# Performance work log

Hardware: AMD Instinct MI355X
Metric: run time of the kernel (lower is better)

The kernel has to match this reference:

```python
import jax, jax.numpy as jnp
import numpy as np

DEGREE = 2
STEPS = 7
N_FEATURES = 120
R_TARGETS = 4
LATENT = 4
D = N_FEATURES + R_TARGETS + LATENT          # 128: padded state dim
N_POLY = 1 + D + D * D                       # 16513: sum_{k=0..degree} D^k for degree=2
BATCH = 16384
W_SCALE = 1e-4                               # keep the iterated quadratic map stable


def setup_inputs() -> dict:
    key = jax.random.key(0)
    k1, k2 = jax.random.split(key)
    X = jax.random.normal(k1, (BATCH, N_FEATURES), dtype=jnp.float32)
    W = jax.random.normal(k2, (N_POLY, D), dtype=jnp.float32) * W_SCALE
    t_init = jnp.zeros((R_TARGETS,), dtype=jnp.float32)
    l_init = jnp.zeros((LATENT,), dtype=jnp.float32)
    return {"X": X, "W": W, "t_init": t_init, "l_init": l_init}


def _poly_full(x):
    """PolynomialFeatures via repeated outer products: [1, x, vec(x xp_{k-1}^T), ...]."""
    n = x.shape[0]
    xp = [jnp.ones((n, 1), x.dtype), x]
    for _ in range(2, DEGREE + 1):
        # [n, D, 1] * [n, 1, P] -> [n, D*P]  (matches tf: X @ expand_dims(XP[-1],1))
        xp.append((x[:, :, None] * xp[-1][:, None, :]).reshape(n, -1))
    return jnp.concatenate(xp, axis=-1)  # [n, N_POLY]


def reference(X, W, t_init, l_init):
    # pad inputs with r_targets + latent_units zeros, then add init values
    inits = jnp.concatenate([jnp.zeros((N_FEATURES,), X.dtype), t_init, l_init])
    x0 = jnp.pad(X, ((0, 0), (0, R_TARGETS + LATENT))) + inits  # [B, D]

    def step(x, _):
        return x + _poly_full(x) @ W, None  # TaylorMap: residual + poly GEMM

    x, _ = jax.lax.scan(step, x0, None, length=STEPS)
    # self._targets = target_features + appended extra target dims
    return x[:, N_FEATURES:N_FEATURES + R_TARGETS]  # [B, n_targets]
```

## Files before the change

### kernel.cpp

```cpp
#include <hip/hip_runtime.h>
#include <hip/hip_bf16.h>


#define DSTATE 128
#define BATCH  16384
#define NSTEPS 7
#define BT     64
#define NSL    585

typedef __attribute__((ext_vector_type(8)))  short  short8;
typedef __attribute__((ext_vector_type(16))) float  f32x16;

__device__ __forceinline__ unsigned short f2bf(float f){
    unsigned int u = __float_as_uint(f);
    u += 0x7fff + ((u >> 16) & 1);
    return (unsigned short)(u >> 16);
}

__global__ void prep_kernel(const float* __restrict__ W, short8* __restrict__ A){
    int gid = blockIdx.x * 256 + threadIdx.x;
    const int ntotal = 4 * 130 * 8 * 64;
    if (gid >= ntotal) return;
    int lane = gid & 63; int r = gid >> 6;
    int s = r & 7;  r >>= 3;
    int row = r % 130;
    int t   = r / 130;
    int d  = t * 32 + (lane & 31);
    int kb = (lane >> 5) * 8;
    int dst;
    bool zero = false;
    if (row < 64){
        int sl = row >> 4;
        if (s < sl) return;
        dst = t * NSL + 9 * row + (s - sl);
    } else if (row < 128){
        int p  = 127 - row;
        int sl = row >> 4;
        if (s < sl) return;
        int ca = 8 - (p >> 4);
        dst = t * NSL + 9 * p + ca + (s - sl);
    } else if (row == 128){
        dst = t * NSL + 576 + s;
    } else {
        if (s) return;
        dst = t * NSL + 584;
        zero = true;
    }
    union { short8 v; unsigned short u[8]; } fr;
#pragma unroll
    for (int e = 0; e < 8; ++e){
        int j = s * 16 + kb + e;
        float v;
        if (zero) v = 0.0f;
        else if (row < 128){
            if      (j < row)  v = 0.0f;
            else if (j == row) v = W[(129 + 128 * row + j) * 128 + d];
            else               v = W[(129 + 128 * row + j) * 128 + d]
                                 + W[(129 + 128 * j + row) * 128 + d];
        } else {
            v = W[(1 + j) * 128 + d];
        }
        fr.u[e] = f2bf(v);
    }
    A[(size_t)dst * 64 + lane] = fr.v;
}

__global__ __launch_bounds__(512)
void taylor_kernel(const float* __restrict__ X, const float* __restrict__ W,
                   const float* __restrict__ tini, const float* __restrict__ lini,
                   const short8* __restrict__ A, float* __restrict__ out)
{
    __shared__ float  x_lds[DSTATE * BT];
    __shared__ float  w0_lds[DSTATE];
    __shared__ short8 bpack[2 * 8 * 64];
    __shared__ float  sc_lds[2][4 * 64 * 17];

    const int tid  = threadIdx.x;
    const int lane = tid & 63;
    const int w    = tid >> 6;
    const int t    = w & 3;
    const int g    = w >> 2;
    const int ln   = lane & 31;
    const int hi   = lane >> 5;
    const int b0   = blockIdx.x * BT;

#pragma unroll
    for (int it = 0; it < 16; ++it){
        int entry = tid + it * 512;
        int b = entry >> 7, d = entry & 127;
        float v;
        if      (d < 120) v = X[(b0 + b) * 120 + d];
        else if (d < 124) v = tini[d - 120];
        else              v = lini[d - 124];
        x_lds[d * BT + b] = v;
    }
    if (tid < DSTATE) w0_lds[tid] = W[tid];

    const short8* const Aw = A + ((size_t)t * NSL + (size_t)g * 288) * 64 + lane;
    const f32x16 zero16 = {};

#pragma unroll 1
    for (int step = 0; step < NSTEPS; ++step){
        __syncthreads();

        const bool active = (step < NSTEPS - 1) || (t == 3);

        const short8* ap = Aw;
        short8 abuf[9];
        if (active){
#pragma unroll
            for (int s = 0; s < 9; ++s) abuf[s] = ap[s * 64];
            ap += 9 * 64;
        }

#pragma unroll
        for (int f0 = 0; f0 < 2; ++f0){
            int f  = tid + f0 * 512;
            int gg = f >> 9, s = (f >> 6) & 7, l = f & 63;
            int c  = gg * 32 + (l & 31);
            int jb = 16 * s + 8 * (l >> 5);
            union { short8 v; unsigned short u[8]; } fr;
#pragma unroll
            for (int e = 0; e < 8; ++e)
                fr.u[e] = f2bf(x_lds[(jb + e) * BT + c]);
            bpack[f] = fr.v;
        }

        f32x16 acc0, acc1;
        if (active){
            if (g == 0){
#pragma unroll
                for (int r = 0; r < 16; ++r){
                    int d = 32 * t + (r & 3) + 8 * (r >> 2) + 4 * hi;
                    acc0[r] = x_lds[d * BT + ln]      + w0_lds[d];
                    acc1[r] = x_lds[d * BT + 32 + ln] + w0_lds[d];
                }
            } else {
#pragma unroll
                for (int r = 0; r < 16; ++r){ acc0[r] = 0.f; acc1[r] = 0.f; }
            }
        }

        __syncthreads();

        if (active){
            short8 bfrag0[8], bfrag1[8];

#define PAIRS(BK)                                                               \
            {                                                                   \
                _Pragma("unroll")                                               \
                for (int s = 0; s < 8 - (BK); ++s){                             \
                    bfrag0[s] = bpack[((BK) + s) * 64 + lane];                  \
                    bfrag1[s] = bpack[512 + ((BK) + s) * 64 + lane];            \
                }                                                               \
                _Pragma("unroll 2")                                             \
                for (int q = 0; q < 16; ++q){                                   \
                    const int p = 16 * (BK) + q;                                \
                    float s0a = x_lds[p * BT + ln];                             \
                    float s0b = x_lds[p * BT + 32 + ln];                        \
                    float s1a = x_lds[(127 - p) * BT + ln];                     \
                    float s1b = x_lds[(127 - p) * BT + 32 + ln];                \
                    f32x16 Y0, Y1;                                              \
                    _Pragma("unroll")                                           \
                    for (int s = 0; s < 8 - (BK); ++s){                         \
                        Y0 = __builtin_amdgcn_mfma_f32_32x32x16_bf16(abuf[s], bfrag0[s], s ? Y0 : zero16, 0, 0, 0); \
                        Y1 = __builtin_amdgcn_mfma_f32_32x32x16_bf16(abuf[s], bfrag1[s], s ? Y1 : zero16, 0, 0, 0); \
                        abuf[s] = ap[s * 64];                                   \
                    }                                                           \
                    acc0 += s0a * Y0;                                           \
                    acc1 += s0b * Y1;                                           \
                    f32x16 Z0, Z1;                                              \
                    _Pragma("unroll")                                           \
                    for (int s = 0; s < 1 + (BK); ++s){                         \
                        Z0 = __builtin_amdgcn_mfma_f32_32x32x16_bf16(abuf[8 - (BK) + s], bfrag0[7 - 2 * (BK) + s], s ? Z0 : zero16, 0, 0, 0); \
                        Z1 = __builtin_amdgcn_mfma_f32_32x32x16_bf16(abuf[8 - (BK) + s], bfrag1[7 - 2 * (BK) + s], s ? Z1 : zero16, 0, 0, 0); \
                        abuf[8 - (BK) + s] = ap[(8 - (BK) + s) * 64];           \
                    }                                                           \
                    acc0 += s1a * Z0;                                           \
                    acc1 += s1b * Z1;                                           \
                    ap += 9 * 64;                                               \
                }                                                               \
            }

            if (g == 0){
                PAIRS(0) PAIRS(1)
            } else {
                PAIRS(2) PAIRS(3)
#pragma unroll
                for (int s = 0; s < 8; ++s){
                    bfrag0[s] = bpack[s * 64 + lane];
                    bfrag1[s] = bpack[512 + s * 64 + lane];
                }
#pragma unroll
                for (int s = 0; s < 8; ++s){
                    acc0 = __builtin_amdgcn_mfma_f32_32x32x16_bf16(abuf[s], bfrag0[s], acc0, 0, 0, 0);
                    acc1 = __builtin_amdgcn_mfma_f32_32x32x16_bf16(abuf[s], bfrag1[s], acc1, 0, 0, 0);
                }
#pragma unroll
                for (int r = 0; r < 16; ++r){
                    sc_lds[0][(t * 64 + lane) * 17 + r] = acc0[r];
                    sc_lds[1][(t * 64 + lane) * 17 + r] = acc1[r];
                }
            }
#undef PAIRS
        }

        __syncthreads();
        if (active && g == 0){
#pragma unroll
            for (int r = 0; r < 16; ++r){
                acc0[r] += sc_lds[0][(t * 64 + lane) * 17 + r];
                acc1[r] += sc_lds[1][(t * 64 + lane) * 17 + r];
            }
            if (step < NSTEPS - 1){
#pragma unroll
                for (int r = 0; r < 16; ++r){
                    int d = 32 * t + (r & 3) + 8 * (r >> 2) + 4 * hi;
                    x_lds[d * BT + ln]      = acc0[r];
                    x_lds[d * BT + 32 + ln] = acc1[r];
                }
            } else if (hi == 0){
                *(float4*)(out + (size_t)(b0 + ln) * 4) =
                    make_float4(acc0[12], acc0[13], acc0[14], acc0[15]);
                *(float4*)(out + (size_t)(b0 + 32 + ln) * 4) =
                    make_float4(acc1[12], acc1[13], acc1[14], acc1[15]);
            }
        }
    }
}

extern "C" void kernel_launch(void* const* d_in, const int* in_sizes, int n_in,
                              void* d_out, int out_size, void* d_ws, size_t ws_size,
                              hipStream_t stream)
{
    const float* X  = (const float*)d_in[0];
    const float* W  = (const float*)d_in[1];
    const float* ti = (const float*)d_in[2];
    const float* li = (const float*)d_in[3];
    float* out      = (float*)d_out;
    short8* A       = (short8*)d_ws;

    const int ntotal = 4 * 130 * 8 * 64;
    prep_kernel<<<(ntotal + 255) / 256, 256, 0, stream>>>(W, A);
    taylor_kernel<<<BATCH / BT, 512, 0, stream>>>(X, W, ti, li, A, out);
}
```

Baseline: 311.3 us.

## Double-buffer A fragments across steps, split final reduction, add MFMA priority hints

Replaces the single A-fragment register buffer with two ping-pong buffers (bufA/bufB) that are prefetched once before the step loop. Each step's last iterations reload the first fragments for the next step, so the global-load latency at step start is hidden. The cross-group reduction is split so each wave group writes one accumulator and finalizes the other, balancing LDS traffic and the epilogue. It also adds s_setprio around the MFMA bursts and launch_bounds(512,2) to request two blocks per CU, which risks register pressure and spills with the doubled buffers.

```diff
diff --git a/kernel.cpp b/kernel.cpp
--- a/kernel.cpp
+++ b/kernel.cpp
@@ -65,7 +65,50 @@
     A[(size_t)dst * 64 + lane] = fr.v;
 }
 
-__global__ __launch_bounds__(512)
+#define QBODY(BK, BUF, pp, RLD)                                                 \
+{                                                                               \
+    const int p_ = (pp);                                                        \
+    float s0a = x_lds[p_ * BT + ln];                                            \
+    float s0b = x_lds[p_ * BT + 32 + ln];                                       \
+    float s1a = x_lds[(127 - p_) * BT + ln];                                    \
+    float s1b = x_lds[(127 - p_) * BT + 32 + ln];                               \
+    f32x16 Y0, Y1;                                                              \
+    __builtin_amdgcn_s_setprio(1);                                              \
+    _Pragma("unroll")                                                           \
+    for (int s = 0; s < 8 - (BK); ++s){                                         \
+        Y0 = __builtin_amdgcn_mfma_f32_32x32x16_bf16(BUF[s], bfrag0[s], s ? Y0 : zero16, 0, 0, 0); \
+        Y1 = __builtin_amdgcn_mfma_f32_32x32x16_bf16(BUF[s], bfrag1[s], s ? Y1 : zero16, 0, 0, 0); \
+        BUF[s] = (RLD)[s * 64];                                                 \
+    }                                                                           \
+    __builtin_amdgcn_s_setprio(0);                                              \
+    acc0 += s0a * Y0;                                                           \
+    acc1 += s0b * Y1;                                                           \
+    f32x16 Z0, Z1;                                                              \
+    __builtin_amdgcn_s_setprio(1);                                              \
+    _Pragma("unroll")                                                           \
+    for (int s = 0; s < 1 + (BK); ++s){                                         \
+        Z0 = __builtin_amdgcn_mfma_f32_32x32x16_bf16(BUF[8 - (BK) + s], bfrag0[7 - 2 * (BK) + s], s ? Z0 : zero16, 0, 0, 0); \
+        Z1 = __builtin_amdgcn_mfma_f32_32x32x16_bf16(BUF[8 - (BK) + s], bfrag1[7 - 2 * (BK) + s], s ? Z1 : zero16, 0, 0, 0); \
+        BUF[8 - (BK) + s] = (RLD)[(8 - (BK) + s) * 64];                         \
+    }                                                                           \
+    __builtin_amdgcn_s_setprio(0);                                              \
+    acc0 += s1a * Z0;                                                           \
+    acc1 += s1b * Z1;                                                           \
+}
+
+#define PAIRS2(BK, NQQ)                                                         \
+    _Pragma("unroll")                                                           \
+    for (int s = 0; s < 8 - (BK); ++s){                                         \
+        bfrag0[s] = bpack[((BK) + s) * 64 + lane];                              \
+        bfrag1[s] = bpack[512 + ((BK) + s) * 64 + lane];                        \
+    }                                                                           \
+    _Pragma("unroll 1")                                                         \
+    for (int qq = 0; qq < (NQQ); ++qq){                                         \
+        QBODY(BK, bufA, 16 * (BK) + 2 * qq,     ap) ap += 9 * 64;               \
+        QBODY(BK, bufB, 16 * (BK) + 2 * qq + 1, ap) ap += 9 * 64;               \
+    }
+
+__global__ __launch_bounds__(512, 2)
 void taylor_kernel(const float* __restrict__ X, const float* __restrict__ W,
                    const float* __restrict__ tini, const float* __restrict__ lini,
                    const short8* __restrict__ A, float* __restrict__ out)
@@ -99,19 +142,18 @@
     const short8* const Aw = A + ((size_t)t * NSL + (size_t)g * 288) * 64 + lane;
     const f32x16 zero16 = {};
 
+    short8 bufA[9], bufB[9];
+#pragma unroll
+    for (int s = 0; s < 9; ++s){
+        bufA[s] = Aw[s * 64];
+        bufB[s] = Aw[(9 + s) * 64];
+    }
+
 #pragma unroll 1
     for (int step = 0; step < NSTEPS; ++step){
         __syncthreads();
 
         const bool active = (step < NSTEPS - 1) || (t == 3);
-
-        const short8* ap = Aw;
-        short8 abuf[9];
-        if (active){
-#pragma unroll
-            for (int s = 0; s < 9; ++s) abuf[s] = ap[s * 64];
-            ap += 9 * 64;
-        }
 
 #pragma unroll
         for (int f0 = 0; f0 < 2; ++f0){
@@ -132,98 +174,89 @@
 #pragma unroll
                 for (int r = 0; r < 16; ++r){
                     int d = 32 * t + (r & 3) + 8 * (r >> 2) + 4 * hi;
-                    acc0[r] = x_lds[d * BT + ln]      + w0_lds[d];
+                    acc0[r] = x_lds[d * BT + ln] + w0_lds[d];
+                    acc1[r] = 0.f;
+                }
+            } else {
+#pragma unroll
+                for (int r = 0; r < 16; ++r){
+                    int d = 32 * t + (r & 3) + 8 * (r >> 2) + 4 * hi;
+                    acc0[r] = 0.f;
                     acc1[r] = x_lds[d * BT + 32 + ln] + w0_lds[d];
                 }
+            }
+        }
+
+        __syncthreads();
+
+        if (active){
+            const short8* ap = Aw + 18 * 64;
+            short8 bfrag0[8], bfrag1[8];
+
+            if (g == 0){
+                PAIRS2(0, 8)
+                PAIRS2(1, 7)
+                QBODY(1, bufA, 30, Aw)
+                QBODY(1, bufB, 31, Aw + 9 * 64)
+#pragma unroll
+                for (int r = 0; r < 16; ++r)
+                    sc_lds[1][(t * 64 + lane) * 17 + r] = acc1[r];
             } else {
-#pragma unroll
-                for (int r = 0; r < 16; ++r){ acc0[r] = 0.f; acc1[r] = 0.f; }
-            }
-        }
-
-        __syncthreads();
-
-        if (active){
-            short8 bfrag0[8], bfrag1[8];
-
-#define PAIRS(BK)                                                               \
-            {                                                                   \
-                _Pragma("unroll")                                               \
-                for (int s = 0; s < 8 - (BK); ++s){                             \
-                    bfrag0[s] = bpack[((BK) + s) * 64 + lane];                  \
-                    bfrag1[s] = bpack[512 + ((BK) + s) * 64 + lane];            \
-                }                                                               \
-                _Pragma("unroll 2")                                             \
-                for (int q = 0; q < 16; ++q){                                   \
-                    const int p = 16 * (BK) + q;                                \
-                    float s0a = x_lds[p * BT + ln];                             \
-                    float s0b = x_lds[p * BT + 32 + ln];                        \
-                    float s1a = x_lds[(127 - p) * BT + ln];                     \
-                    float s1b = x_lds[(127 - p) * BT + 32 + ln];                \
-                    f32x16 Y0, Y1;                                              \
-                    _Pragma("unroll")                                           \
-                    for (int s = 0; s < 8 - (BK); ++s){                         \
-                        Y0 = __builtin_amdgcn_mfma_f32_32x32x16_bf16(abuf[s], bfrag0[s], s ? Y0 : zero16, 0, 0, 0); \
-                        Y1 = __builtin_amdgcn_mfma_f32_32x32x16_bf16(abuf[s], bfrag1[s], s ? Y1 : zero16, 0, 0, 0); \
-                        abuf[s] = ap[s * 64];                                   \
-                    }                                                           \
-                    acc0 += s0a * Y0;                                           \
-                    acc1 += s0b * Y1;                                           \
-                    f32x16 Z0, Z1;                                              \
-                    _Pragma("unroll")                                           \
-                    for (int s = 0; s < 1 + (BK); ++s){                         \
-                        Z0 = __builtin_amdgcn_mfma_f32_32x32x16_bf16(abuf[8 - (BK) + s], bfrag0[7 - 2 * (BK) + s], s ? Z0 : zero16, 0, 0, 0); \
-                        Z1 = __builtin_amdgcn_mfma_f32_32x32x16_bf16(abuf[8 - (BK) + s], bfrag1[7 - 2 * (BK) + s], s ? Z1 : zero16, 0, 0, 0); \
-                        abuf[8 - (BK) + s] = ap[(8 - (BK) + s) * 64];           \
-                    }                                                           \
-                    acc0 += s1a * Z0;                                           \
-                    acc1 += s1b * Z1;                                           \
-                    ap += 9 * 64;                                               \
-                }                                                               \
-            }
-
-            if (g == 0){
-                PAIRS(0) PAIRS(1)
-            } else {
-                PAIRS(2) PAIRS(3)
+                PAIRS2(2, 8)
+                PAIRS2(3, 7)
+                QBODY(3, bufA, 62, ap)
+                QBODY(3, bufB, 63, Aw + 9 * 64)
 #pragma unroll
                 for (int s = 0; s < 8; ++s){
                     bfrag0[s] = bpack[s * 64 + lane];
                     bfrag1[s] = bpack[512 + s * 64 + lane];
                 }
+                __builtin_amdgcn_s_setprio(1);
 #pragma unroll
                 for (int s = 0; s < 8; ++s){
-                    acc0 = __builtin_amdgcn_mfma_f32_32x32x16_bf16(abuf[s], bfrag0[s], acc0, 0, 0, 0);
-                    acc1 = __builtin_amdgcn_mfma_f32_32x32x16_bf16(abuf[s], bfrag1[s], acc1, 0, 0, 0);
-                }
-#pragma unroll
-                for (int r = 0; r < 16; ++r){
+                    acc0 = __builtin_amdgcn_mfma_f32_32x32x16_bf16(bufA[s], bfrag0[s], acc0, 0, 0, 0);
+                    acc1 = __builtin_amdgcn_mfma_f32_32x32x16_bf16(bufA[s], bfrag1[s], acc1, 0, 0, 0);
+                }
+                __builtin_amdgcn_s_setprio(0);
+#pragma unroll
+                for (int s = 0; s < 9; ++s) bufA[s] = Aw[s * 64];
+#pragma unroll
+                for (int r = 0; r < 16; ++r)
                     sc_lds[0][(t * 64 + lane) * 17 + r] = acc0[r];
-                    sc_lds[1][(t * 64 + lane) * 17 + r] = acc1[r];
-                }
             }
-#undef PAIRS
         }
 
         __syncthreads();
-        if (active && g == 0){
-#pragma unroll
-            for (int r = 0; r < 16; ++r){
-                acc0[r] += sc_lds[0][(t * 64 + lane) * 17 + r];
-                acc1[r] += sc_lds[1][(t * 64 + lane) * 17 + r];
-            }
-            if (step < NSTEPS - 1){
-#pragma unroll
-                for (int r = 0; r < 16; ++r){
-                    int d = 32 * t + (r & 3) + 8 * (r >> 2) + 4 * hi;
-                    x_lds[d * BT + ln]      = acc0[r];
-                    x_lds[d * BT + 32 + ln] = acc1[r];
-                }
-            } else if (hi == 0){
-                *(float4*)(out + (size_t)(b0 + ln) * 4) =
-                    make_float4(acc0[12], acc0[13], acc0[14], acc0[15]);
-                *(float4*)(out + (size_t)(b0 + 32 + ln) * 4) =
-                    make_float4(acc1[12], acc1[13], acc1[14], acc1[15]);
+
+        if (active){
+            if (g == 0){
+#pragma unroll
+                for (int r = 0; r < 16; ++r)
+                    acc0[r] += sc_lds[0][(t * 64 + lane) * 17 + r];
+                if (step < NSTEPS - 1){
+#pragma unroll
+                    for (int r = 0; r < 16; ++r){
+                        int d = 32 * t + (r & 3) + 8 * (r >> 2) + 4 * hi;
+                        x_lds[d * BT + ln] = acc0[r];
+                    }
+                } else if (hi == 0){
+                    *(float4*)(out + (size_t)(b0 + ln) * 4) =
+                        make_float4(acc0[12], acc0[13], acc0[14], acc0[15]);
+                }
+            } else {
+#pragma unroll
+                for (int r = 0; r < 16; ++r)
+                    acc1[r] += sc_lds[1][(t * 64 + lane) * 17 + r];
+                if (step < NSTEPS - 1){
+#pragma unroll
+                    for (int r = 0; r < 16; ++r){
+                        int d = 32 * t + (r & 3) + 8 * (r >> 2) + 4 * hi;
+                        x_lds[d * BT + 32 + ln] = acc1[r];
+                    }
+                } else if (hi == 0){
+                    *(float4*)(out + (size_t)(b0 + 32 + ln) * 4) =
+                        make_float4(acc1[12], acc1[13], acc1[14], acc1[15]);
+                }
             }
         }
     }
```

Result: slower. 494.5 us (+58.9%).

## Balance split-K reduction across wave groups and raise MFMA issue priority

Applied to the files above, without the earlier changes.

The group-1 waves now run the linear-term MFMAs first, then the quadratic pairs. Each wave group writes half of its partial accumulators to LDS and finalizes the other half, so the reduction and state writeback are split between both groups instead of done by group 0 alone. s_setprio brackets are added around the MFMA chains so waves with matrix work are favoured by the scheduler. This is meant to shorten the serialized epilogue after the barrier, at the cost of more branching and register pressure.

```diff
diff --git a/kernel.cpp b/kernel.cpp
--- a/kernel.cpp
+++ b/kernel.cpp
@@ -96,7 +96,8 @@
     }
     if (tid < DSTATE) w0_lds[tid] = W[tid];
 
-    const short8* const Aw = A + ((size_t)t * NSL + (size_t)g * 288) * 64 + lane;
+    const short8* const Aw   = A + ((size_t)t * NSL + (size_t)g * 288) * 64 + lane;
+    const short8* const Alin = A + ((size_t)t * NSL + 576) * 64 + lane;
     const f32x16 zero16 = {};
 
 #pragma unroll 1
@@ -108,9 +109,14 @@
         const short8* ap = Aw;
         short8 abuf[9];
         if (active){
-#pragma unroll
-            for (int s = 0; s < 9; ++s) abuf[s] = ap[s * 64];
-            ap += 9 * 64;
+            if (g == 0){
+#pragma unroll
+                for (int s = 0; s < 9; ++s) abuf[s] = ap[s * 64];
+                ap += 9 * 64;
+            } else {
+#pragma unroll
+                for (int s = 0; s < 9; ++s) abuf[s] = Alin[s * 64];
+            }
         }
 
 #pragma unroll
@@ -132,12 +138,16 @@
 #pragma unroll
                 for (int r = 0; r < 16; ++r){
                     int d = 32 * t + (r & 3) + 8 * (r >> 2) + 4 * hi;
-                    acc0[r] = x_lds[d * BT + ln]      + w0_lds[d];
+                    acc0[r] = x_lds[d * BT + ln] + w0_lds[d];
+                    acc1[r] = 0.f;
+                }
+            } else {
+#pragma unroll
+                for (int r = 0; r < 16; ++r){
+                    int d = 32 * t + (r & 3) + 8 * (r >> 2) + 4 * hi;
+                    acc0[r] = 0.f;
                     acc1[r] = x_lds[d * BT + 32 + ln] + w0_lds[d];
                 }
-            } else {
-#pragma unroll
-                for (int r = 0; r < 16; ++r){ acc0[r] = 0.f; acc1[r] = 0.f; }
             }
         }
 
@@ -161,21 +171,25 @@
                     float s1a = x_lds[(127 - p) * BT + ln];                     \
                     float s1b = x_lds[(127 - p) * BT + 32 + ln];                \
                     f32x16 Y0, Y1;                                              \
+                    __builtin_amdgcn_s_setprio(1);                              \
                     _Pragma("unroll")                                           \
                     for (int s = 0; s < 8 - (BK); ++s){                         \
                         Y0 = __builtin_amdgcn_mfma_f32_32x32x16_bf16(abuf[s], bfrag0[s], s ? Y0 : zero16, 0, 0, 0); \
                         Y1 = __builtin_amdgcn_mfma_f32_32x32x16_bf16(abuf[s], bfrag1[s], s ? Y1 : zero16, 0, 0, 0); \
                         abuf[s] = ap[s * 64];                                   \
                     }                                                           \
+                    __builtin_amdgcn_s_setprio(0);                              \
                     acc0 += s0a * Y0;                                           \
                     acc1 += s0b * Y1;                                           \
                     f32x16 Z0, Z1;                                              \
+                    __builtin_amdgcn_s_setprio(1);                              \
                     _Pragma("unroll")                                           \
                     for (int s = 0; s < 1 + (BK); ++s){                         \
                         Z0 = __builtin_amdgcn_mfma_f32_32x32x16_bf16(abuf[8 - (BK) + s], bfrag0[7 - 2 * (BK) + s], s ? Z0 : zero16, 0, 0, 0); \
                         Z1 = __builtin_amdgcn_mfma_f32_32x32x16_bf16(abuf[8 - (BK) + s], bfrag1[7 - 2 * (BK) + s], s ? Z1 : zero16, 0, 0, 0); \
                         abuf[8 - (BK) + s] = ap[(8 - (BK) + s) * 64];           \
                     }                                                           \
+                    __builtin_amdgcn_s_setprio(0);                              \
                     acc0 += s1a * Z0;                                           \
                     acc1 += s1b * Z1;                                           \
                     ap += 9 * 64;                                               \
@@ -184,46 +198,64 @@
 
             if (g == 0){
                 PAIRS(0) PAIRS(1)
-            } else {
-                PAIRS(2) PAIRS(3)
+#pragma unroll
+                for (int r = 0; r < 16; ++r)
+                    sc_lds[1][(t * 64 + lane) * 17 + r] = acc1[r];
+            } else {
 #pragma unroll
                 for (int s = 0; s < 8; ++s){
                     bfrag0[s] = bpack[s * 64 + lane];
                     bfrag1[s] = bpack[512 + s * 64 + lane];
                 }
+                __builtin_amdgcn_s_setprio(1);
 #pragma unroll
                 for (int s = 0; s < 8; ++s){
                     acc0 = __builtin_amdgcn_mfma_f32_32x32x16_bf16(abuf[s], bfrag0[s], acc0, 0, 0, 0);
                     acc1 = __builtin_amdgcn_mfma_f32_32x32x16_bf16(abuf[s], bfrag1[s], acc1, 0, 0, 0);
-                }
-#pragma unroll
-                for (int r = 0; r < 16; ++r){
+                    abuf[s] = Aw[s * 64];
+                }
+                __builtin_amdgcn_s_setprio(0);
+                abuf[8] = Aw[8 * 64];
+                ap = Aw + 9 * 64;
+                PAIRS(2) PAIRS(3)
+#pragma unroll
+                for (int r = 0; r < 16; ++r)
                     sc_lds[0][(t * 64 + lane) * 17 + r] = acc0[r];
-                    sc_lds[1][(t * 64 + lane) * 17 + r] = acc1[r];
-                }
             }
 #undef PAIRS
         }
 
         __syncthreads();
-        if (active && g == 0){
-#pragma unroll
-            for (int r = 0; r < 16; ++r){
-                acc0[r] += sc_lds[0][(t * 64 + lane) * 17 + r];
-                acc1[r] += sc_lds[1][(t * 64 + lane) * 17 + r];
-            }
-            if (step < NSTEPS - 1){
-#pragma unroll
-                for (int r = 0; r < 16; ++r){
-                    int d = 32 * t + (r & 3) + 8 * (r >> 2) + 4 * hi;
-                    x_lds[d * BT + ln]      = acc0[r];
-                    x_lds[d * BT + 32 + ln] = acc1[r];
-                }
-            } else if (hi == 0){
-                *(float4*)(out + (size_t)(b0 + ln) * 4) =
-                    make_float4(acc0[12], acc0[13], acc0[14], acc0[15]);
-                *(float4*)(out + (size_t)(b0 + 32 + ln) * 4) =
-                    make_float4(acc1[12], acc1[13], acc1[14], acc1[15]);
+
+        if (active){
+            if (g == 0){
+#pragma unroll
+                for (int r = 0; r < 16; ++r)
+                    acc0[r] += sc_lds[0][(t * 64 + lane) * 17 + r];
+                if (step < NSTEPS - 1){
+#pragma unroll
+                    for (int r = 0; r < 16; ++r){
+                        int d = 32 * t + (r & 3) + 8 * (r >> 2) + 4 * hi;
+                        x_lds[d * BT + ln] = acc0[r];
+                    }
+                } else if (hi == 0){
+                    *(float4*)(out + (size_t)(b0 + ln) * 4) =
+                        make_float4(acc0[12], acc0[13], acc0[14], acc0[15]);
+                }
+            } else {
+#pragma unroll
+                for (int r = 0; r < 16; ++r)
+                    acc1[r] += sc_lds[1][(t * 64 + lane) * 17 + r];
+                if (step < NSTEPS - 1){
+#pragma unroll
+                    for (int r = 0; r < 16; ++r){
+                        int d = 32 * t + (r & 3) + 8 * (r >> 2) + 4 * hi;
+                        x_lds[d * BT + 32 + ln] = acc1[r];
+                    }
+                } else if (hi == 0){
+                    *(float4*)(out + (size_t)(b0 + 32 + ln) * 4) =
+                        make_float4(acc1[12], acc1[13], acc1[14], acc1[15]);
+                }
             }
         }
     }
```

Measured after the change: 321.8 us. +3.4%, slower.

## Stream A fragments through LDS ring via global_load_lds double buffering

Applied to the files above, without the earlier changes.

Moves four of the nine per-iteration A-fragment loads from register-resident global loads to asynchronous global_load_lds transfers into a per-wave double-buffered LDS ring, with explicit vmcnt waits. Barriers become s_waitcnt lgkmcnt plus s_barrier. The aim is to cut VGPR pressure and hide global-load latency behind the MFMA chains. In exchange it adds LDS traffic and reads, and depends on fragile hand-tuned vmcnt counts being correct.

```diff
diff --git a/kernel.cpp b/kernel.cpp
--- a/kernel.cpp
+++ b/kernel.cpp
@@ -16,6 +16,15 @@
     u += 0x7fff + ((u >> 16) & 1);
     return (unsigned short)(u >> 16);
 }
+
+__device__ __forceinline__ void barrier_lgkm(){
+    asm volatile("s_waitcnt lgkmcnt(0)" ::: "memory");
+    __builtin_amdgcn_s_barrier();
+}
+
+#define GLL(gp, lp) __builtin_amdgcn_global_load_lds(                           \
+        (const __attribute__((address_space(1))) void*)(gp),                    \
+        (__attribute__((address_space(3))) void*)(lp), 16, 0, 0)
 
 __global__ void prep_kernel(const float* __restrict__ W, short8* __restrict__ A){
     int gid = blockIdx.x * 256 + threadIdx.x;
@@ -74,6 +83,7 @@
     __shared__ float  w0_lds[DSTATE];
     __shared__ short8 bpack[2 * 8 * 64];
     __shared__ float  sc_lds[2][4 * 64 * 17];
+    __shared__ short8 ring[8][2][4][64];
 
     const int tid  = threadIdx.x;
     const int lane = tid & 63;
@@ -99,9 +109,14 @@
     const short8* const Aw = A + ((size_t)t * NSL + (size_t)g * 288) * 64 + lane;
     const f32x16 zero16 = {};
 
+    const short8* const rring0 = &ring[w][0][0][lane];
+    const short8* const rring1 = &ring[w][1][0][lane];
+    char* const rdst0 = (char*)&ring[w][0][0][0];
+    char* const rdst1 = (char*)&ring[w][1][0][0];
+
 #pragma unroll 1
     for (int step = 0; step < NSTEPS; ++step){
-        __syncthreads();
+        barrier_lgkm();
 
         const bool active = (step < NSTEPS - 1) || (t == 3);
 
@@ -109,8 +124,15 @@
         short8 abuf[9];
         if (active){
 #pragma unroll
-            for (int s = 0; s < 9; ++s) abuf[s] = ap[s * 64];
-            ap += 9 * 64;
+            for (int s2 = 0; s2 < 4; ++s2)
+                GLL(Aw + s2 * 64, rdst0 + s2 * 1024);
+            asm volatile("" ::: "memory");
+#pragma unroll
+            for (int s = 4; s < 9; ++s) abuf[s] = Aw[s * 64];
+#pragma unroll
+            for (int s2 = 0; s2 < 4; ++s2)
+                GLL(Aw + (9 + s2) * 64, rdst1 + s2 * 1024);
+            ap = Aw + 9 * 64;
         }
 
 #pragma unroll
@@ -141,12 +163,12 @@
             }
         }
 
-        __syncthreads();
+        barrier_lgkm();
 
         if (active){
             short8 bfrag0[8], bfrag1[8];
 
-#define PAIRS(BK)                                                               \
+#define PAIRS(BK, NQ, LASTB)                                                    \
             {                                                                   \
                 _Pragma("unroll")                                               \
                 for (int s = 0; s < 8 - (BK); ++s){                             \
@@ -154,18 +176,30 @@
                     bfrag1[s] = bpack[512 + ((BK) + s) * 64 + lane];            \
                 }                                                               \
                 _Pragma("unroll 2")                                             \
-                for (int q = 0; q < 16; ++q){                                   \
+                for (int q = 0; q < (NQ); ++q){                                 \
                     const int p = 16 * (BK) + q;                                \
+                    asm volatile("s_waitcnt vmcnt(9)" ::: "memory");            \
+                    const short8* rp = ((p) & 1) ? rring1 : rring0;             \
+                    abuf[0] = rp[0];   abuf[1] = rp[64];                        \
+                    abuf[2] = rp[128]; abuf[3] = rp[192];                       \
                     float s0a = x_lds[p * BT + ln];                             \
                     float s0b = x_lds[p * BT + 32 + ln];                        \
                     float s1a = x_lds[(127 - p) * BT + ln];                     \
                     float s1b = x_lds[(127 - p) * BT + 32 + ln];                \
                     f32x16 Y0, Y1;                                              \
+                    Y0 = __builtin_amdgcn_mfma_f32_32x32x16_bf16(abuf[4], bfrag0[4], zero16, 0, 0, 0); \
+                    Y1 = __builtin_amdgcn_mfma_f32_32x32x16_bf16(abuf[4], bfrag1[4], zero16, 0, 0, 0); \
+                    abuf[4] = ap[4 * 64];                                       \
                     _Pragma("unroll")                                           \
-                    for (int s = 0; s < 8 - (BK); ++s){                         \
-                        Y0 = __builtin_amdgcn_mfma_f32_32x32x16_bf16(abuf[s], bfrag0[s], s ? Y0 : zero16, 0, 0, 0); \
-                        Y1 = __builtin_amdgcn_mfma_f32_32x32x16_bf16(abuf[s], bfrag1[s], s ? Y1 : zero16, 0, 0, 0); \
+                    for (int s = 5; s < 8 - (BK); ++s){                         \
+                        Y0 = __builtin_amdgcn_mfma_f32_32x32x16_bf16(abuf[s], bfrag0[s], Y0, 0, 0, 0); \
+                        Y1 = __builtin_amdgcn_mfma_f32_32x32x16_bf16(abuf[s], bfrag1[s], Y1, 0, 0, 0); \
                         abuf[s] = ap[s * 64];                                   \
+                    }                                                           \
+                    _Pragma("unroll")                                           \
+                    for (int s = 0; s < 4; ++s){                                \
+                        Y0 = __builtin_amdgcn_mfma_f32_32x32x16_bf16(abuf[s], bfrag0[s], Y0, 0, 0, 0); \
+                        Y1 = __builtin_amdgcn_mfma_f32_32x32x16_bf16(abuf[s], bfrag1[s], Y1, 0, 0, 0); \
                     }                                                           \
                     acc0 += s0a * Y0;                                           \
                     acc1 += s0b * Y1;                                           \
@@ -178,14 +212,31 @@
                     }                                                           \
                     acc0 += s1a * Z0;                                           \
                     acc1 += s1b * Z1;                                           \
+                    {                                                           \
+                        \
+                        \
+                        \
+                        \
+                        const short8* gsrc = ((LASTB) && q == (NQ) - 1)         \
+                                           ? Aw : (ap + 9 * 64);                \
+                        char* ldst = ((p) & 1) ? rdst1 : rdst0;                 \
+                        _Pragma("unroll")                                       \
+                        for (int s2 = 0; s2 < 4; ++s2)                          \
+                            GLL(gsrc + s2 * 64, ldst + s2 * 1024);              \
+                    }                                                           \
                     ap += 9 * 64;                                               \
                 }                                                               \
             }
 
             if (g == 0){
-                PAIRS(0) PAIRS(1)
+                PAIRS(0, 16, 0)
+                PAIRS(1, 16, 0)
             } else {
-                PAIRS(2) PAIRS(3)
+                PAIRS(2, 16, 0)
+                PAIRS(3, 16, 1)
+                asm volatile("s_waitcnt vmcnt(9)" ::: "memory");
+                abuf[0] = rring0[0];   abuf[1] = rring0[64];
+                abuf[2] = rring0[128]; abuf[3] = rring0[192];
 #pragma unroll
                 for (int s = 0; s < 8; ++s){
                     bfrag0[s] = bpack[s * 64 + lane];
@@ -205,7 +256,7 @@
 #undef PAIRS
         }
 
-        __syncthreads();
+        barrier_lgkm();
         if (active && g == 0){
 #pragma unroll
             for (int r = 0; r < 16; ++r){
```

Result: slower. 331.3 us (+6.4%).
